# Kernel optimization log

Measured on AMD Instinct MI355X. Metric: run time of the kernel, lower is better.

Reference implementation:

```python
import jax, jax.numpy as jnp
import numpy as np
import math

EMBED_LEN = 128  # dk, head dim

def setup_inputs() -> dict:
    key = jax.random.key(0)
    kq, kk, kv = jax.random.split(key, 3)
    shape = (2, 16, 2048, EMBED_LEN)  # [batch, heads, seq, head_dim]
    return {
        "queries": jax.random.normal(kq, shape, dtype=jnp.float32),
        "keys": jax.random.normal(kk, shape, dtype=jnp.float32),
        "values": jax.random.normal(kv, shape, dtype=jnp.float32),
    }

def reference(queries, keys, values):
    # compatibility = Q @ K^T / sqrt(dk); softmax over last dim; then @ V
    scale = 1.0 / math.sqrt(EMBED_LEN)
    scores = jnp.einsum("bhqd,bhkd->bhqk", queries, keys) * scale
    attn = jax.nn.softmax(scores, axis=-1)
    # mask is None in init, so no tril applied (matches original)
    return jnp.einsum("bhqk,bhkd->bhqd", attn, values)
```

## Files before the change

### kernel.cpp

```cpp
#include <hip/hip_runtime.h>

typedef float  f32x4  __attribute__((ext_vector_type(4)));
typedef float  f32x16 __attribute__((ext_vector_type(16)));
typedef short  s16x8  __attribute__((ext_vector_type(8)));
typedef unsigned short u16x4 __attribute__((ext_vector_type(4)));

#define SEQ   2048
#define DH    128
#define BM    128
#define BN    64
#define NT    (SEQ/BN)

__device__ __forceinline__ unsigned short f2bf(float x){
  unsigned u = __builtin_bit_cast(unsigned, x);
  return (unsigned short)((u + 0x8000u) >> 16);
}

__global__ __launch_bounds__(256, 2)
void sdpa_fwd(const float* __restrict__ Qg, const float* __restrict__ Kg,
              const float* __restrict__ Vg, float* __restrict__ Og)
{
  __shared__ char kbuf[16384];
  __shared__ char vbuf[16384];
  __shared__ char pbuf[16384];

  const int tid = threadIdx.x;
  const int w   = tid >> 6;
  const int l   = tid & 63;
  const int h2  = l >> 5;
  const int ln  = l & 31;
  const int c4  = tid & 31;
  const int rq  = tid >> 5;

  const int bid = (int)blockIdx.x;
  const int bh  = ((bid & 7) << 2) | ((bid >> 3) & 3);
  const int qt  = bid >> 5;

  const size_t base = (size_t)bh * (SEQ*DH);
  const float* Qb = Qg + base;
  const float* Kb = Kg + base;
  const float* Vb = Vg + base;
  float*       Ob = Og + base;

  const int qrow = qt*BM + w*32 + ln;
  const float scale = 0.08838834764831845f;

  s16x8 qf[8];
#pragma unroll
  for (int kc = 0; kc < 8; ++kc) {
    const float* p = Qb + (size_t)qrow*DH + kc*16 + h2*8;
    f32x4 a = *(const f32x4*)p;
    f32x4 b = *(const f32x4*)(p+4);
    s16x8 r;
    r[0] = (short)f2bf(a[0]*scale); r[1] = (short)f2bf(a[1]*scale);
    r[2] = (short)f2bf(a[2]*scale); r[3] = (short)f2bf(a[3]*scale);
    r[4] = (short)f2bf(b[0]*scale); r[5] = (short)f2bf(b[1]*scale);
    r[6] = (short)f2bf(b[2]*scale); r[7] = (short)f2bf(b[3]*scale);
    qf[kc] = r;
  }

  f32x16 ot[4];
#pragma unroll
  for (int dt = 0; dt < 4; ++dt)
#pragma unroll
    for (int r = 0; r < 16; ++r) ot[dt][r] = 0.f;

  float m_run = -1e30f, l_run = 0.f;

  f32x4 kst[8], vst[8];

  auto fetch = [&](int t) {
    const int kv0 = t * BN;
#pragma unroll
    for (int kk = 0; kk < 8; ++kk)
      kst[kk] = *(const f32x4*)(Kb + (size_t)(kv0 + rq + kk*8)*DH + c4*4);
#pragma unroll
    for (int it = 0; it < 2; ++it)
#pragma unroll
      for (int i = 0; i < 4; ++i)
        vst[it*4+i] = *(const f32x4*)(Vb + (size_t)(kv0 + (rq + it*8)*4 + i)*DH + c4*4);
  };

  fetch(0);

  for (int t = 0; t < NT; ++t) {
    __syncthreads();

#pragma unroll
    for (int kk = 0; kk < 8; ++kk) {
      const int kv  = rq + kk*8;
      const int mm  = kv >> 5, r31 = kv & 31;
      const int kc  = c4 >> 2, hh = (c4 >> 1) & 1;
      const int Wk  = (2*kc + hh) & 7;
      const int byt = (((mm*8 + kc)*2 + hh) << 9) | ((r31 ^ Wk) << 4) | ((c4 & 1) << 3);
      u16x4 v;
      v[0] = f2bf(kst[kk][0]); v[1] = f2bf(kst[kk][1]);
      v[2] = f2bf(kst[kk][2]); v[3] = f2bf(kst[kk][3]);
      *(u16x4*)(kbuf + byt) = v;
    }
#pragma unroll
    for (int it = 0; it < 2; ++it) {
      const int rqp = rq + it*8;
      const int ks  = rqp >> 2, hp = (rqp >> 1) & 1, j0b = (rqp & 1) << 3;
#pragma unroll
      for (int ii = 0; ii < 4; ++ii) {
        const int dt  = c4 >> 3;
        const int d31 = ((c4 & 7) << 2) | ii;
        const int Wv  = (2*dt + hp) & 7;
        const int byt = (((ks*4 + dt)*2 + hp) << 9) | ((d31 ^ Wv) << 4) | j0b;
        u16x4 v;
        v[0] = f2bf(vst[it*4+0][ii]); v[1] = f2bf(vst[it*4+1][ii]);
        v[2] = f2bf(vst[it*4+2][ii]); v[3] = f2bf(vst[it*4+3][ii]);
        *(u16x4*)(vbuf + byt) = v;
      }
    }
    if (t + 1 < NT) fetch(t + 1);
    __syncthreads();

    f32x16 sa[2];
#pragma unroll
    for (int mm = 0; mm < 2; ++mm) {
#pragma unroll
      for (int r = 0; r < 16; ++r) sa[mm][r] = 0.f;
#pragma unroll
      for (int kc = 0; kc < 8; ++kc) {
        const int byt = (((mm*8 + kc)*2 + h2) << 9) | ((ln ^ ((2*kc + h2) & 7)) << 4);
        s16x8 a = *(const s16x8*)(kbuf + byt);
        sa[mm] = __builtin_amdgcn_mfma_f32_32x32x16_bf16(a, qf[kc], sa[mm], 0, 0, 0);
      }
    }

    float tmax = sa[0][0];
#pragma unroll
    for (int mm = 0; mm < 2; ++mm)
#pragma unroll
      for (int r = 0; r < 16; ++r) tmax = fmaxf(tmax, sa[mm][r]);
    tmax = fmaxf(tmax, __shfl_xor(tmax, 32));
    const float mnew  = fmaxf(m_run, tmax);
    const float alpha = __expf(m_run - mnew);
    float psum = 0.f;
    const int wbase = w << 12;
#pragma unroll
    for (int mm = 0; mm < 2; ++mm)
#pragma unroll
      for (int tq = 0; tq < 4; ++tq) {
        u16x4 pk;
#pragma unroll
        for (int rr = 0; rr < 4; ++rr) {
          const float pv = __expf(sa[mm][tq*4+rr] - mnew);
          psum += pv;
          pk[rr] = f2bf(pv);
        }
        const int byt = wbase | (ln << 7) | ((mm*64 + tq*16 + h2*8) ^ ((ln & 7) << 4));
        *(u16x4*)(pbuf + byt) = pk;
      }
    psum += __shfl_xor(psum, 32);
    l_run = l_run * alpha + psum;
    m_run = mnew;
#pragma unroll
    for (int dt = 0; dt < 4; ++dt)
#pragma unroll
      for (int r = 0; r < 16; ++r) ot[dt][r] *= alpha;

    asm volatile("s_waitcnt lgkmcnt(0)" ::: "memory");
    __builtin_amdgcn_sched_barrier(0);

#pragma unroll
    for (int ks = 0; ks < 4; ++ks) {
      const int pbyt = wbase | (ln << 7) | ((ks*32 + h2*16) ^ ((ln & 7) << 4));
      s16x8 pb = *(const s16x8*)(pbuf + pbyt);
#pragma unroll
      for (int dt = 0; dt < 4; ++dt) {
        const int vbyt = (((ks*4 + dt)*2 + h2) << 9) | ((ln ^ ((2*dt + h2) & 7)) << 4);
        s16x8 va = *(const s16x8*)(vbuf + vbyt);
        ot[dt] = __builtin_amdgcn_mfma_f32_32x32x16_bf16(va, pb, ot[dt], 0, 0, 0);
      }
    }
  }

  const float inv = 1.0f / l_run;
#pragma unroll
  for (int dt = 0; dt < 4; ++dt)
#pragma unroll
    for (int tq = 0; tq < 4; ++tq) {
      f32x4 o;
      o[0] = ot[dt][tq*4+0]*inv; o[1] = ot[dt][tq*4+1]*inv;
      o[2] = ot[dt][tq*4+2]*inv; o[3] = ot[dt][tq*4+3]*inv;
      const int d0 = dt*32 + tq*8 + h2*4;
      *(f32x4*)(Ob + (size_t)qrow*DH + d0) = o;
    }
}

extern "C" void kernel_launch(void* const* d_in, const int* in_sizes, int n_in,
                              void* d_out, int out_size, void* d_ws, size_t ws_size,
                              hipStream_t stream)
{
  (void)in_sizes; (void)n_in; (void)d_ws; (void)ws_size; (void)out_size;
  const float* Q = (const float*)d_in[0];
  const float* K = (const float*)d_in[1];
  const float* V = (const float*)d_in[2];
  float* O = (float*)d_out;
  dim3 grid(512), block(256);
  hipLaunchKernelGGL(sdpa_fwd, grid, block, 0, stream, Q, K, V, O);
}
```

Baseline: 216.8 us.

## Pre-convert K/V to bf16, split KV across warp halves, async LDS loads

Adds two pre-pass kernels that convert K to bf16 and V to a transposed bf16 layout in workspace. The attention kernel then streams these tiles into LDS with global_load_lds double-buffering, which removes per-tile register staging and conversion. Each block of 512 threads splits the KV sequence between two warp halves and merges their partial softmax states at the end. It also keeps P in registers through permlane32 swaps instead of an LDS round trip, uses exp2 with a log2e-folded scale, and skips the rescale unless the running max grows by more than 8. The cost is extra kernel launches, extra global traffic for the converted copies, and larger LDS use per block.

Measured after the change: 295.0 us. 36.0% more time.

```diff
diff --git a/kernel.cpp b/kernel.cpp
--- a/kernel.cpp
+++ b/kernel.cpp
@@ -3,203 +3,228 @@
 typedef float  f32x4  __attribute__((ext_vector_type(4)));
 typedef float  f32x16 __attribute__((ext_vector_type(16)));
 typedef short  s16x8  __attribute__((ext_vector_type(8)));
-typedef unsigned short u16x4 __attribute__((ext_vector_type(4)));
-
-#define SEQ   2048
-#define DH    128
-#define BM    128
-#define BN    64
-#define NT    (SEQ/BN)
-
-__device__ __forceinline__ unsigned short f2bf(float x){
-  unsigned u = __builtin_bit_cast(unsigned, x);
-  return (unsigned short)((u + 0x8000u) >> 16);
-}
-
-__global__ __launch_bounds__(256, 2)
-void sdpa_fwd(const float* __restrict__ Qg, const float* __restrict__ Kg,
-              const float* __restrict__ Vg, float* __restrict__ Og)
+typedef unsigned u32x2 __attribute__((ext_vector_type(2)));
+typedef int    i32x4  __attribute__((ext_vector_type(4)));
+
+#define SEQ 2048
+#define DH  128
+#define BN  32
+#define NTILE 32
+
+__device__ __forceinline__ unsigned pk2bf(float a, float b){
+  union { __bf16 h[2]; unsigned u; } x;
+  x.h[0] = (__bf16)a; x.h[1] = (__bf16)b; return x.u;
+}
+
+__device__ __forceinline__ void gl16(const unsigned short* g, void* s){
+  __builtin_amdgcn_global_load_lds(
+      (const __attribute__((address_space(1))) void*)g,
+      (__attribute__((address_space(3))) void*)s, 16, 0, 0);
+}
+
+__global__ __launch_bounds__(256) void cvt_k(const float* __restrict__ in,
+                                             unsigned short* __restrict__ out){
+  size_t id = (size_t)blockIdx.x*256 + threadIdx.x;
+  f32x4 v = *(const f32x4*)(in + id*4);
+  u32x2 o; o[0] = pk2bf(v[0], v[1]); o[1] = pk2bf(v[2], v[3]);
+  *(u32x2*)(out + id*4) = o;
+}
+
+__global__ __launch_bounds__(256) void cvt_vt(const float* __restrict__ V,
+                                              unsigned short* __restrict__ Vt){
+  __shared__ float tile[32][33];
+  const int bid = blockIdx.x;
+  const int bh = bid >> 8, t5 = bid & 255;
+  const int kv0 = (t5 >> 2) * 32, d0 = (t5 & 3) * 32;
+  const int r = threadIdx.x >> 3, c = (threadIdx.x & 7) * 4;
+  f32x4 v = *(const f32x4*)(V + ((size_t)bh*SEQ + kv0 + r)*DH + d0 + c);
+  tile[r][c+0]=v[0]; tile[r][c+1]=v[1]; tile[r][c+2]=v[2]; tile[r][c+3]=v[3];
+  __syncthreads();
+  u32x2 o;
+  o[0] = pk2bf(tile[c+0][r], tile[c+1][r]);
+  o[1] = pk2bf(tile[c+2][r], tile[c+3][r]);
+  *(u32x2*)(Vt + ((size_t)bh*DH + d0 + r)*SEQ + kv0 + c) = o;
+}
+
+__global__ __launch_bounds__(512, 4)
+void sdpa_fwd(const float* __restrict__ Qg, const unsigned short* __restrict__ Kbf,
+              const unsigned short* __restrict__ Vtb, float* __restrict__ Og)
 {
-  __shared__ char kbuf[16384];
-  __shared__ char vbuf[16384];
-  __shared__ char pbuf[16384];
+  __shared__ __align__(16) char smem[68608];
 
   const int tid = threadIdx.x;
-  const int w   = tid >> 6;
-  const int l   = tid & 63;
-  const int h2  = l >> 5;
-  const int ln  = l & 31;
-  const int c4  = tid & 31;
-  const int rq  = tid >> 5;
+  const int w = tid >> 6, l = tid & 63, ln = l & 31, h2 = l >> 5;
+  const int half = w >> 2, pair = w & 3;
 
   const int bid = (int)blockIdx.x;
-  const int bh  = ((bid & 7) << 2) | ((bid >> 3) & 3);
-  const int qt  = bid >> 5;
-
-  const size_t base = (size_t)bh * (SEQ*DH);
-  const float* Qb = Qg + base;
-  const float* Kb = Kg + base;
-  const float* Vb = Vg + base;
-  float*       Ob = Og + base;
-
-  const int qrow = qt*BM + w*32 + ln;
-  const float scale = 0.08838834764831845f;
+  const int bh = ((bid & 7) << 2) | ((bid >> 3) & 3);
+  const int qt = bid >> 5;
+
+  const float* Qb = Qg + (size_t)bh*(SEQ*DH);
+  const unsigned short* Kb = Kbf + (size_t)bh*(SEQ*DH);
+  const unsigned short* Vb = Vtb + (size_t)bh*(SEQ*DH);
+  float* Ob = Og + (size_t)bh*(SEQ*DH);
+
+  const int qrow = qt*128 + pair*32 + ln;
+  const float qsc = 0.1275174156f;
 
   s16x8 qf[8];
 #pragma unroll
   for (int kc = 0; kc < 8; ++kc) {
     const float* p = Qb + (size_t)qrow*DH + kc*16 + h2*8;
-    f32x4 a = *(const f32x4*)p;
-    f32x4 b = *(const f32x4*)(p+4);
-    s16x8 r;
-    r[0] = (short)f2bf(a[0]*scale); r[1] = (short)f2bf(a[1]*scale);
-    r[2] = (short)f2bf(a[2]*scale); r[3] = (short)f2bf(a[3]*scale);
-    r[4] = (short)f2bf(b[0]*scale); r[5] = (short)f2bf(b[1]*scale);
-    r[6] = (short)f2bf(b[2]*scale); r[7] = (short)f2bf(b[3]*scale);
-    qf[kc] = r;
-  }
+    f32x4 a = *(const f32x4*)p, b = *(const f32x4*)(p+4);
+    i32x4 t;
+    t[0] = (int)pk2bf(a[0]*qsc, a[1]*qsc);
+    t[1] = (int)pk2bf(a[2]*qsc, a[3]*qsc);
+    t[2] = (int)pk2bf(b[0]*qsc, b[1]*qsc);
+    t[3] = (int)pk2bf(b[2]*qsc, b[3]*qsc);
+    qf[kc] = __builtin_bit_cast(s16x8, t);
+  }
+
+  const int i0 = pair, i1 = pair + 4;
+  const unsigned short* kg0 = Kb + ((size_t)(half*1024) + (ln ^ ((2*i0+h2)&7)))*DH + 16*i0 + 8*h2;
+  const unsigned short* kg1 = Kb + ((size_t)(half*1024) + (ln ^ ((2*i1+h2)&7)))*DH + 16*i1 + 8*h2;
+  const unsigned short* vg0 = Vb + (size_t)(32*(i0&3) + (ln ^ ((2*(i0&3)+h2)&7)))*SEQ
+                                 + half*1024 + 16*(i0>>2) + 8*h2;
+  const unsigned short* vg1 = Vb + (size_t)(32*(i1&3) + (ln ^ ((2*(i1&3)+h2)&7)))*SEQ
+                                 + half*1024 + 16*(i1>>2) + 8*h2;
 
   f32x16 ot[4];
 #pragma unroll
   for (int dt = 0; dt < 4; ++dt)
 #pragma unroll
     for (int r = 0; r < 16; ++r) ot[dt][r] = 0.f;
-
   float m_run = -1e30f, l_run = 0.f;
 
-  f32x4 kst[8], vst[8];
-
-  auto fetch = [&](int t) {
-    const int kv0 = t * BN;
-#pragma unroll
-    for (int kk = 0; kk < 8; ++kk)
-      kst[kk] = *(const f32x4*)(Kb + (size_t)(kv0 + rq + kk*8)*DH + c4*4);
-#pragma unroll
-    for (int it = 0; it < 2; ++it)
-#pragma unroll
-      for (int i = 0; i < 4; ++i)
-        vst[it*4+i] = *(const f32x4*)(Vb + (size_t)(kv0 + (rq + it*8)*4 + i)*DH + c4*4);
+  auto issue = [&](int t, int db) {
+    char* base = smem + (size_t)(half*2 + db)*16384;
+    gl16(kg0 + (size_t)t*(BN*DH), base + i0*1024);
+    gl16(kg1 + (size_t)t*(BN*DH), base + i1*1024);
+    gl16(vg0 + t*BN, base + 8192 + i0*1024);
+    gl16(vg1 + t*BN, base + 8192 + i1*1024);
   };
 
-  fetch(0);
-
-  for (int t = 0; t < NT; ++t) {
-    __syncthreads();
-
-#pragma unroll
-    for (int kk = 0; kk < 8; ++kk) {
-      const int kv  = rq + kk*8;
-      const int mm  = kv >> 5, r31 = kv & 31;
-      const int kc  = c4 >> 2, hh = (c4 >> 1) & 1;
-      const int Wk  = (2*kc + hh) & 7;
-      const int byt = (((mm*8 + kc)*2 + hh) << 9) | ((r31 ^ Wk) << 4) | ((c4 & 1) << 3);
-      u16x4 v;
-      v[0] = f2bf(kst[kk][0]); v[1] = f2bf(kst[kk][1]);
-      v[2] = f2bf(kst[kk][2]); v[3] = f2bf(kst[kk][3]);
-      *(u16x4*)(kbuf + byt) = v;
-    }
-#pragma unroll
-    for (int it = 0; it < 2; ++it) {
-      const int rqp = rq + it*8;
-      const int ks  = rqp >> 2, hp = (rqp >> 1) & 1, j0b = (rqp & 1) << 3;
-#pragma unroll
-      for (int ii = 0; ii < 4; ++ii) {
-        const int dt  = c4 >> 3;
-        const int d31 = ((c4 & 7) << 2) | ii;
-        const int Wv  = (2*dt + hp) & 7;
-        const int byt = (((ks*4 + dt)*2 + hp) << 9) | ((d31 ^ Wv) << 4) | j0b;
-        u16x4 v;
-        v[0] = f2bf(vst[it*4+0][ii]); v[1] = f2bf(vst[it*4+1][ii]);
-        v[2] = f2bf(vst[it*4+2][ii]); v[3] = f2bf(vst[it*4+3][ii]);
-        *(u16x4*)(vbuf + byt) = v;
-      }
-    }
-    if (t + 1 < NT) fetch(t + 1);
-    __syncthreads();
-
-    f32x16 sa[2];
-#pragma unroll
-    for (int mm = 0; mm < 2; ++mm) {
-#pragma unroll
-      for (int r = 0; r < 16; ++r) sa[mm][r] = 0.f;
-#pragma unroll
-      for (int kc = 0; kc < 8; ++kc) {
-        const int byt = (((mm*8 + kc)*2 + h2) << 9) | ((ln ^ ((2*kc + h2) & 7)) << 4);
-        s16x8 a = *(const s16x8*)(kbuf + byt);
-        sa[mm] = __builtin_amdgcn_mfma_f32_32x32x16_bf16(a, qf[kc], sa[mm], 0, 0, 0);
-      }
-    }
-
-    float tmax = sa[0][0];
-#pragma unroll
-    for (int mm = 0; mm < 2; ++mm)
-#pragma unroll
-      for (int r = 0; r < 16; ++r) tmax = fmaxf(tmax, sa[mm][r]);
+  issue(0, 0);
+  __syncthreads();
+
+  int db = 0;
+  for (int t = 0; t < NTILE; ++t) {
+    if (t + 1 < NTILE) issue(t + 1, db ^ 1);
+    const char* base = smem + (size_t)(half*2 + db)*16384;
+
+    f32x16 sa;
+#pragma unroll
+    for (int r = 0; r < 16; ++r) sa[r] = 0.f;
+#pragma unroll
+    for (int kc = 0; kc < 8; ++kc) {
+      const int frag = 2*kc + h2;
+      s16x8 a = *(const s16x8*)(base + frag*512 + ((ln ^ (frag & 7)) << 4));
+      sa = __builtin_amdgcn_mfma_f32_32x32x16_bf16(a, qf[kc], sa, 0, 0, 0);
+    }
+
+    float tmax = fmaxf(sa[0], sa[1]);
+#pragma unroll
+    for (int r = 2; r < 16; ++r) tmax = fmaxf(tmax, sa[r]);
     tmax = fmaxf(tmax, __shfl_xor(tmax, 32));
-    const float mnew  = fmaxf(m_run, tmax);
-    const float alpha = __expf(m_run - mnew);
+    if (!__all(tmax <= m_run + 8.f)) {
+      const float mnew = fmaxf(m_run, tmax);
+      const float al = __builtin_amdgcn_exp2f(m_run - mnew);
+      l_run *= al;
+#pragma unroll
+      for (int dt = 0; dt < 4; ++dt)
+#pragma unroll
+        for (int r = 0; r < 16; ++r) ot[dt][r] *= al;
+      m_run = mnew;
+    }
     float psum = 0.f;
-    const int wbase = w << 12;
-#pragma unroll
-    for (int mm = 0; mm < 2; ++mm)
-#pragma unroll
-      for (int tq = 0; tq < 4; ++tq) {
-        u16x4 pk;
-#pragma unroll
-        for (int rr = 0; rr < 4; ++rr) {
-          const float pv = __expf(sa[mm][tq*4+rr] - mnew);
-          psum += pv;
-          pk[rr] = f2bf(pv);
-        }
-        const int byt = wbase | (ln << 7) | ((mm*64 + tq*16 + h2*8) ^ ((ln & 7) << 4));
-        *(u16x4*)(pbuf + byt) = pk;
-      }
+#pragma unroll
+    for (int r = 0; r < 16; ++r) {
+      sa[r] = __builtin_amdgcn_exp2f(sa[r] - m_run);
+      psum += sa[r];
+    }
     psum += __shfl_xor(psum, 32);
-    l_run = l_run * alpha + psum;
-    m_run = mnew;
-#pragma unroll
-    for (int dt = 0; dt < 4; ++dt)
-#pragma unroll
-      for (int r = 0; r < 16; ++r) ot[dt][r] *= alpha;
-
-    asm volatile("s_waitcnt lgkmcnt(0)" ::: "memory");
-    __builtin_amdgcn_sched_barrier(0);
-
-#pragma unroll
-    for (int ks = 0; ks < 4; ++ks) {
-      const int pbyt = wbase | (ln << 7) | ((ks*32 + h2*16) ^ ((ln & 7) << 4));
-      s16x8 pb = *(const s16x8*)(pbuf + pbyt);
+    l_run += psum;
+
+    i32x4 pw[2];
+#pragma unroll
+    for (int ks = 0; ks < 2; ++ks) {
+      unsigned x0 = pk2bf(sa[8*ks+0], sa[8*ks+1]);
+      unsigned x1 = pk2bf(sa[8*ks+2], sa[8*ks+3]);
+      unsigned y0 = pk2bf(sa[8*ks+4], sa[8*ks+5]);
+      unsigned y1 = pk2bf(sa[8*ks+6], sa[8*ks+7]);
+      u32x2 s0 = __builtin_amdgcn_permlane32_swap(x0, y0, false, false);
+      u32x2 s1 = __builtin_amdgcn_permlane32_swap(x1, y1, false, false);
+      i32x4 b; b[0] = (int)s0[0]; b[1] = (int)s1[0]; b[2] = (int)s0[1]; b[3] = (int)s1[1];
+      pw[ks] = b;
+    }
+
+#pragma unroll
+    for (int ks = 0; ks < 2; ++ks) {
+      s16x8 pb = __builtin_bit_cast(s16x8, pw[ks]);
 #pragma unroll
       for (int dt = 0; dt < 4; ++dt) {
-        const int vbyt = (((ks*4 + dt)*2 + h2) << 9) | ((ln ^ ((2*dt + h2) & 7)) << 4);
-        s16x8 va = *(const s16x8*)(vbuf + vbyt);
+        const int frag = 2*(ks*4 + dt) + h2;
+        s16x8 va = *(const s16x8*)(base + 8192 + frag*512 + ((ln ^ (frag & 7)) << 4));
         ot[dt] = __builtin_amdgcn_mfma_f32_32x32x16_bf16(va, pb, ot[dt], 0, 0, 0);
       }
     }
-  }
-
-  const float inv = 1.0f / l_run;
-#pragma unroll
-  for (int dt = 0; dt < 4; ++dt)
-#pragma unroll
-    for (int tq = 0; tq < 4; ++tq) {
-      f32x4 o;
-      o[0] = ot[dt][tq*4+0]*inv; o[1] = ot[dt][tq*4+1]*inv;
-      o[2] = ot[dt][tq*4+2]*inv; o[3] = ot[dt][tq*4+3]*inv;
-      const int d0 = dt*32 + tq*8 + h2*4;
-      *(f32x4*)(Ob + (size_t)qrow*DH + d0) = o;
-    }
+
+    __syncthreads();
+    db ^= 1;
+  }
+
+  float* obuf = (float*)smem;
+  float* mbuf = (float*)(smem + 67584);
+  float* lbuf = (float*)(smem + 68096);
+  if (half == 1) {
+    mbuf[pair*32 + ln] = m_run;
+    lbuf[pair*32 + ln] = l_run;
+    float* orow = obuf + (size_t)(pair*32 + ln)*132;
+#pragma unroll
+    for (int dt = 0; dt < 4; ++dt)
+#pragma unroll
+      for (int rq = 0; rq < 4; ++rq) {
+        f32x4 v;
+        v[0] = ot[dt][rq*4+0]; v[1] = ot[dt][rq*4+1];
+        v[2] = ot[dt][rq*4+2]; v[3] = ot[dt][rq*4+3];
+        *(f32x4*)(orow + dt*32 + rq*8 + h2*4) = v;
+      }
+  }
+  __syncthreads();
+  if (half == 0) {
+    const float m1 = mbuf[pair*32 + ln], l1 = lbuf[pair*32 + ln];
+    const float ms = fmaxf(m_run, m1);
+    const float a0 = __builtin_amdgcn_exp2f(m_run - ms);
+    const float a1 = __builtin_amdgcn_exp2f(m1 - ms);
+    const float inv = 1.f / (l_run*a0 + l1*a1);
+    const float s0 = a0*inv, s1 = a1*inv;
+    const float* orow = obuf + (size_t)(pair*32 + ln)*132;
+#pragma unroll
+    for (int dt = 0; dt < 4; ++dt)
+#pragma unroll
+      for (int rq = 0; rq < 4; ++rq) {
+        f32x4 o1 = *(const f32x4*)(orow + dt*32 + rq*8 + h2*4);
+        f32x4 o;
+#pragma unroll
+        for (int k = 0; k < 4; ++k) o[k] = ot[dt][rq*4+k]*s0 + o1[k]*s1;
+        *(f32x4*)(Ob + (size_t)qrow*DH + dt*32 + rq*8 + h2*4) = o;
+      }
+  }
 }
 
 extern "C" void kernel_launch(void* const* d_in, const int* in_sizes, int n_in,
                               void* d_out, int out_size, void* d_ws, size_t ws_size,
                               hipStream_t stream)
 {
-  (void)in_sizes; (void)n_in; (void)d_ws; (void)ws_size; (void)out_size;
+  (void)in_sizes; (void)n_in; (void)out_size; (void)ws_size;
   const float* Q = (const float*)d_in[0];
   const float* K = (const float*)d_in[1];
   const float* V = (const float*)d_in[2];
   float* O = (float*)d_out;
-  dim3 grid(512), block(256);
-  hipLaunchKernelGGL(sdpa_fwd, grid, block, 0, stream, Q, K, V, O);
-}
+  unsigned short* Kbf = (unsigned short*)d_ws;
+  unsigned short* Vt  = Kbf + (size_t)32*SEQ*DH;
+
+  hipLaunchKernelGGL(cvt_k,  dim3(8192), dim3(256), 0, stream, K, Kbf);
+  hipLaunchKernelGGL(cvt_vt, dim3(8192), dim3(256), 0, stream, V, Vt);
+  hipLaunchKernelGGL(sdpa_fwd, dim3(512), dim3(512), 0, stream, Q, Kbf, Vt, O);
+}
```
